# Optimization experiments

Hardware: AMD Instinct MI355X
Metric: run time of the kernel (lower is better)

The kernel has to match this reference:

```python
import jax, jax.numpy as jnp
import numpy as np

B, S, HID = 1, 8192, 768
H, D = 12, 64          # num heads, head dim (HID = H*D)
W = 256                # one-sided attention window


def _shift_chunks(xc, C):
    # xc: [B, C, w, H, D] -> prev/next chunk copies padded with zeros
    prev = jnp.pad(xc, ((0, 0), (1, 0), (0, 0), (0, 0), (0, 0)))[:, :C]
    nxt = jnp.pad(xc, ((0, 0), (0, 1), (0, 0), (0, 0), (0, 0)))[:, 1:]
    return jnp.concatenate([prev, xc, nxt], axis=2)  # [B, C, 3w, H, D]


def sliding_window_attention(q, k, v, w):
    # q,k,v: [B, S, H, D]; q already scaled. Band width 2w+1.
    b, s, h, d = q.shape
    c = s // w
    qc = q.reshape(b, c, w, h, d)
    k3 = _shift_chunks(k.reshape(b, c, w, h, d), c)  # [b,c,3w,h,d]
    v3 = _shift_chunks(v.reshape(b, c, w, h, d), c)
    # scores of each query chunk against its 3-chunk key neighborhood
    scores3 = jnp.einsum('bcxhd,bcyhd->bhcxy', qc, k3)  # [b,h,c,w,3w]
    rows = jnp.arange(w)
    offs = jnp.arange(2 * w + 1)
    gidx = rows[:, None] + offs[None, :]  # [w, 2w+1] local key index p+j
    band = scores3[..., rows[:, None], gidx]  # [b,h,c,w,2w+1]
    # mask keys outside [0, S) (same effect as mask_invalid_locations)
    gq = jnp.arange(s).reshape(c, w)                    # global query pos
    keypos = gq[..., None] + (offs - w)                 # [c,w,2w+1]
    valid = (keypos >= 0) & (keypos < s)
    band = jnp.where(valid[None, None], band, -jnp.inf)
    prob = jax.nn.softmax(band, axis=-1)
    prob = jnp.where(valid[None, None], prob, 0.0)
    # scatter band probs back to 3w layout, then banded PV matmul
    prob3 = jnp.zeros(band.shape[:-1] + (3 * w,), band.dtype)
    prob3 = prob3.at[..., rows[:, None], gidx].set(prob)  # [b,h,c,w,3w]
    ctx = jnp.einsum('bhcxy,bcyhd->bcxhd', prob3, v3)
    return ctx.reshape(b, s, h, d)


def setup_inputs() -> dict:
    key = jax.random.key(0)
    ks = jax.random.split(key, 4)
    sc = 1.0 / np.sqrt(HID)
    return {
        'hidden_states': jax.random.normal(ks[0], (B, S, HID), jnp.float32),
        'Wq': jax.random.normal(ks[1], (HID, HID), jnp.float32) * sc,
        'bq': jnp.zeros((HID,), jnp.float32),
        'Wk': jax.random.normal(ks[2], (HID, HID), jnp.float32) * sc,
        'bk': jnp.zeros((HID,), jnp.float32),
        'Wv': jax.random.normal(ks[3], (HID, HID), jnp.float32) * sc,
        'bv': jnp.zeros((HID,), jnp.float32),
    }


def reference(hidden_states, Wq, bq, Wk, bk, Wv, bv):
    b, s, hid = hidden_states.shape
    q = (hidden_states @ Wq + bq).reshape(b, s, H, D)
    k = (hidden_states @ Wk + bk).reshape(b, s, H, D)
    v = (hidden_states @ Wv + bv).reshape(b, s, H, D)
    q = q / jnp.asarray(np.sqrt(D), q.dtype)
    ctx = sliding_window_attention(q, k, v, W)  # [b,s,H,D]
    return ctx.reshape(b, s, hid)
```

## Files before the change

### kernel.cpp

```cpp
#include <hip/hip_runtime.h>
#include <hip/hip_bf16.h>

#define S_LEN 8192
#define HID 768
#define NH 12
#define HD 64
#define WIN 256

typedef __bf16 bf16x8 __attribute__((ext_vector_type(8)));
typedef float f32x4 __attribute__((ext_vector_type(4)));
using bf16_t = __hip_bfloat16;

#define MFMA(a, b, c) __builtin_amdgcn_mfma_f32_16x16x32_bf16(a, b, c, 0, 0, 0)

__device__ __forceinline__ void gl2lds16(const bf16_t* g, bf16_t* l) {
  __builtin_amdgcn_global_load_lds(
      (const __attribute__((address_space(1))) void*)g,
      (__attribute__((address_space(3))) void*)l, 16, 0, 0);
}

__global__ __launch_bounds__(256) void conv_hs(const float* __restrict__ hs,
                                               bf16_t* __restrict__ hb) {
  int i = (blockIdx.x * 256 + threadIdx.x) * 4;
  float4 v = *reinterpret_cast<const float4*>(hs + i);
  union { ushort4 u; bf16_t b[4]; } H;
  H.b[0] = __float2bfloat16(v.x);
  H.b[1] = __float2bfloat16(v.y);
  H.b[2] = __float2bfloat16(v.z);
  H.b[3] = __float2bfloat16(v.w);
  *reinterpret_cast<ushort4*>(hb + i) = H.u;
}

__global__ __launch_bounds__(256) void transpose_w(const float* __restrict__ Wq,
                                                   const float* __restrict__ Wk,
                                                   const float* __restrict__ Wv,
                                                   bf16_t* __restrict__ Wt) {
  __shared__ float t[32][33];
  int z = blockIdx.z;
  const float* src = (z == 0) ? Wq : ((z == 1) ? Wk : Wv);
  int n0 = blockIdx.x * 32, k0 = blockIdx.y * 32;
  int tx = threadIdx.x, ty = threadIdx.y;
  for (int i = 0; i < 4; ++i)
    t[ty + i * 8][tx] = src[(k0 + ty + i * 8) * HID + n0 + tx];
  __syncthreads();
  bf16_t* dst = Wt + z * HID * HID;
  for (int i = 0; i < 4; ++i)
    dst[(n0 + ty + i * 8) * HID + k0 + tx] = __float2bfloat16(t[tx][ty + i * 8]);
}

__global__ __launch_bounds__(256) void qkv_gemm(
    const bf16_t* __restrict__ hb, const bf16_t* __restrict__ Wt,
    const float* __restrict__ bq, const float* __restrict__ bk,
    const float* __restrict__ bv,
    bf16_t* __restrict__ Qw, bf16_t* __restrict__ Kw, bf16_t* __restrict__ Vt) {
  __shared__ __align__(16) bf16_t sA[128 * 64];
  __shared__ __align__(16) bf16_t sB[128 * 64];
  int m0 = blockIdx.x * 128;
  int zq = blockIdx.y / 6;
  int nn0 = (blockIdx.y % 6) * 128;
  int n0g = zq * HID + nn0;
  int tid = threadIdx.x;
  int w = tid >> 6, lane = tid & 63, lm = lane & 15, qd = lane >> 4;
  int wm = w & 1, wn = w >> 1;

  int srow = w * 8 + (lane >> 3);
  int sc8 = (lane & 7) ^ ((lane >> 3) & 7);
  const bf16_t* gA = hb + (m0 + srow) * HID + sc8 * 8;
  const bf16_t* gB = Wt + (n0g + srow) * HID + sc8 * 8;
  int sx0 = lm & 7;

  f32x4 acc[4][4] = {};
  for (int kk = 0; kk < HID; kk += 64) {
#pragma unroll
    for (int u = 0; u < 4; ++u) {
      gl2lds16(gA + (u * 32) * HID + kk, sA + u * 2048 + w * 512);
      gl2lds16(gB + (u * 32) * HID + kk, sB + u * 2048 + w * 512);
    }
    __syncthreads();
#pragma unroll
    for (int half = 0; half < 2; ++half) {
      int ca = (qd + 4 * half) ^ sx0;
      bf16x8 fa[4], fb[4];
#pragma unroll
      for (int i = 0; i < 4; ++i) {
        fa[i] = *reinterpret_cast<const bf16x8*>(
            sA + (wm * 64 + i * 16 + lm) * 64 + ca * 8);
        fb[i] = *reinterpret_cast<const bf16x8*>(
            sB + (wn * 64 + i * 16 + lm) * 64 + ca * 8);
      }
      if (zq == 2) {
#pragma unroll
        for (int i = 0; i < 4; ++i)
#pragma unroll
          for (int j = 0; j < 4; ++j)
            acc[i][j] = MFMA(fb[i], fa[j], acc[i][j]);
      } else {
#pragma unroll
        for (int i = 0; i < 4; ++i)
#pragma unroll
          for (int j = 0; j < 4; ++j)
            acc[i][j] = MFMA(fa[i], fb[j], acc[i][j]);
      }
    }
    __syncthreads();
  }

  if (zq != 2) {
    const float* bias = zq ? bk : bq;
    bf16_t* dst = zq ? Kw : Qw;
    float scale = zq ? 1.0f : 0.125f;
#pragma unroll
    for (int j = 0; j < 4; ++j) {
      int nl = nn0 + wn * 64 + j * 16 + lm;
      float bb = bias[nl];
      int h = nl >> 6, d = nl & 63;
#pragma unroll
      for (int i = 0; i < 4; ++i)
#pragma unroll
        for (int r = 0; r < 4; ++r) {
          int m = m0 + wm * 64 + i * 16 + qd * 4 + r;
          dst[(h * S_LEN + m) * HD + d] =
              __float2bfloat16((acc[i][j][r] + bb) * scale);
        }
    }
  } else {
#pragma unroll
    for (int i = 0; i < 4; ++i)
#pragma unroll
      for (int r = 0; r < 4; ++r) {
        int nl = nn0 + wn * 64 + i * 16 + qd * 4 + r;
        float bb = bv[nl];
#pragma unroll
        for (int j = 0; j < 4; ++j) {
          int m = m0 + wm * 64 + j * 16 + lm;
          Vt[nl * S_LEN + m] = __float2bfloat16(acc[i][j][r] + bb);
        }
      }
  }
}

__global__ __launch_bounds__(256) void swa_kernel(
    const bf16_t* __restrict__ Qw, const bf16_t* __restrict__ Kw,
    const bf16_t* __restrict__ Vt, float* __restrict__ out) {
  __shared__ __align__(16) bf16_t sK[2][64 * 64];
  __shared__ __align__(16) bf16_t sV[2][64 * 64];
  __shared__ __align__(16) bf16_t sP[4 * 16 * 72];
  int h = blockIdx.y;
  int nb = blockIdx.x;
  int q0 = (((nb & 7) << 4) | (nb >> 3)) * 64;
  int tid = threadIdx.x;
  int w = tid >> 6, lane = tid & 63, lm = lane & 15, qd = lane >> 4;
  int xb = q0 + w * 16;

  int qoff = (h * S_LEN + xb + lm) * HD + qd * 8;
  bf16x8 aq0 = *reinterpret_cast<const bf16x8*>(Qw + qoff);
  bf16x8 aq1 = *reinterpret_cast<const bf16x8*>(Qw + qoff + 32);

  f32x4 o[4] = {};
  float lsum[4] = {0.f, 0.f, 0.f, 0.f};

  int y_begin = q0 - WIN; if (y_begin < 0) y_begin = 0;
  int y_end = q0 + 64 + WIN; if (y_end > S_LEN) y_end = S_LEN;
  int ntiles = (y_end - y_begin) >> 6;
  const bf16_t* Kh = Kw + h * S_LEN * HD;
  const bf16_t* Vh = Vt + h * HD * S_LEN;
  bf16_t* sPw = sP + w * 16 * 72;

  int srow = w * 8 + (lane >> 3);
  int sc8 = (lane & 7) ^ ((lane >> 3) & 7);
  int sx0 = lm & 7;

#define STAGE(y0, b)                                                    \
  {                                                                     \
    const bf16_t* kg = Kh + ((y0) + srow) * HD + sc8 * 8;               \
    gl2lds16(kg, &sK[b][w * 512]);                                      \
    gl2lds16(kg + 32 * HD, &sK[b][2048 + w * 512]);                     \
    const bf16_t* vg = Vh + srow * S_LEN + (y0) + sc8 * 8;              \
    gl2lds16(vg, &sV[b][w * 512]);                                      \
    gl2lds16(vg + 32 * S_LEN, &sV[b][2048 + w * 512]);                  \
  }

  STAGE(y_begin, 0);
  __syncthreads();

  for (int t = 0; t < ntiles; ++t) {
    int y0 = y_begin + t * 64;
    if (t + 1 < ntiles) STAGE(y0 + 64, (t + 1) & 1);
    int b = t & 1;
    f32x4 s[4] = {};
#pragma unroll
    for (int nt = 0; nt < 4; ++nt) {
      const bf16_t* kr = &sK[b][(nt * 16 + lm) * 64];
      bf16x8 b0 = *reinterpret_cast<const bf16x8*>(kr + (qd ^ sx0) * 8);
      bf16x8 b1 = *reinterpret_cast<const bf16x8*>(kr + ((qd + 4) ^ sx0) * 8);
      s[nt] = MFMA(aq0, b0, s[nt]);
      s[nt] = MFMA(aq1, b1, s[nt]);
    }
    int dy = y0 - q0;
    bool edge = (dy > 192) || (dy < -192);
#pragma unroll
    for (int nt = 0; nt < 4; ++nt) {
#pragma unroll
      for (int r = 0; r < 4; ++r) {
        float pv;
        if (edge) {
          int dlt = (y0 + nt * 16 + lm) - (xb + qd * 4 + r);
          pv = (dlt <= WIN && dlt >= -WIN) ? __expf(s[nt][r]) : 0.f;
        } else {
          pv = __expf(s[nt][r]);
        }
        bf16_t pb = __float2bfloat16(pv);
        lsum[r] += __bfloat162float(pb);
        sPw[(qd * 4 + r) * 72 + nt * 16 + lm] = pb;
      }
    }
    bf16x8 ap0 = *reinterpret_cast<const bf16x8*>(sPw + lm * 72 + qd * 8);
    bf16x8 ap1 = *reinterpret_cast<const bf16x8*>(sPw + lm * 72 + 32 + qd * 8);
#pragma unroll
    for (int nt = 0; nt < 4; ++nt) {
      const bf16_t* vr = &sV[b][(nt * 16 + lm) * 64];
      bf16x8 v0 = *reinterpret_cast<const bf16x8*>(vr + (qd ^ sx0) * 8);
      bf16x8 v1 = *reinterpret_cast<const bf16x8*>(vr + ((qd + 4) ^ sx0) * 8);
      o[nt] = MFMA(ap0, v0, o[nt]);
      o[nt] = MFMA(ap1, v1, o[nt]);
    }
    __syncthreads();
  }
#pragma unroll
  for (int r = 0; r < 4; ++r) {
    float v = lsum[r];
    v += __shfl_xor(v, 1);
    v += __shfl_xor(v, 2);
    v += __shfl_xor(v, 4);
    v += __shfl_xor(v, 8);
    float inv = 1.f / v;
    int x = xb + qd * 4 + r;
#pragma unroll
    for (int nt = 0; nt < 4; ++nt)
      out[x * HID + h * HD + nt * 16 + lm] = o[nt][r] * inv;
  }
}

extern "C" void kernel_launch(void* const* d_in, const int* in_sizes, int n_in,
                              void* d_out, int out_size, void* d_ws, size_t ws_size,
                              hipStream_t stream) {
  const float* hs = (const float*)d_in[0];
  const float* Wq = (const float*)d_in[1];
  const float* bq = (const float*)d_in[2];
  const float* Wk = (const float*)d_in[3];
  const float* bk = (const float*)d_in[4];
  const float* Wv = (const float*)d_in[5];
  const float* bv = (const float*)d_in[6];
  float* out = (float*)d_out;

  const int NSH = S_LEN * HID;
  const int NW = 3 * HID * HID;
  bf16_t* p = (bf16_t*)d_ws;
  bf16_t* hb = p; p += NSH;
  bf16_t* Wt = p; p += NW;
  bf16_t* Qw = p; p += NSH;
  bf16_t* Kw = p; p += NSH;
  bf16_t* Vt = p; p += NSH;

  conv_hs<<<dim3(NSH / 4 / 256), dim3(256), 0, stream>>>(hs, hb);
  transpose_w<<<dim3(24, 24, 3), dim3(32, 8), 0, stream>>>(Wq, Wk, Wv, Wt);
  qkv_gemm<<<dim3(64, 18), dim3(256), 0, stream>>>(
      hb, Wt, bq, bk, bv, Qw, Kw, Vt);
  swa_kernel<<<dim3(128, 12), dim3(256), 0, stream>>>(Qw, Kw, Vt, out);
}
```

Before: 175.1 us.

## Merge prep kernels and transpose QK^T MFMA for vectorized P stores

Combines the hidden-state bf16 conversion and the weight transpose into one launch, which removes a kernel launch. In the attention kernel, the QK^T MFMA operands are swapped so each lane holds scores for one query row. This lets P be written to LDS as packed 4-element stores with an XOR swizzle instead of scalar stores with padding. The row sum becomes a single accumulator reduced across quads. It also adds a launch-bounds occupancy hint and sums unrounded fp32 probabilities, which changes numerics slightly.

```diff
diff --git a/kernel.cpp b/kernel.cpp
--- a/kernel.cpp
+++ b/kernel.cpp
@@ -19,27 +19,32 @@
       (__attribute__((address_space(3))) void*)l, 16, 0, 0);
 }
 
-__global__ __launch_bounds__(256) void conv_hs(const float* __restrict__ hs,
-                                               bf16_t* __restrict__ hb) {
-  int i = (blockIdx.x * 256 + threadIdx.x) * 4;
-  float4 v = *reinterpret_cast<const float4*>(hs + i);
-  union { ushort4 u; bf16_t b[4]; } H;
-  H.b[0] = __float2bfloat16(v.x);
-  H.b[1] = __float2bfloat16(v.y);
-  H.b[2] = __float2bfloat16(v.z);
-  H.b[3] = __float2bfloat16(v.w);
-  *reinterpret_cast<ushort4*>(hb + i) = H.u;
-}
-
-__global__ __launch_bounds__(256) void transpose_w(const float* __restrict__ Wq,
-                                                   const float* __restrict__ Wk,
-                                                   const float* __restrict__ Wv,
-                                                   bf16_t* __restrict__ Wt) {
+__global__ __launch_bounds__(256) void prep(const float* __restrict__ hs,
+                                            bf16_t* __restrict__ hb,
+                                            const float* __restrict__ Wq,
+                                            const float* __restrict__ Wk,
+                                            const float* __restrict__ Wv,
+                                            bf16_t* __restrict__ Wt) {
+  int bx = blockIdx.x;
+  int tid = threadIdx.x;
+  if (bx < 6144) {
+    int i = (bx * 256 + tid) * 4;
+    float4 v = *reinterpret_cast<const float4*>(hs + i);
+    union { ushort4 u; bf16_t b[4]; } H;
+    H.b[0] = __float2bfloat16(v.x);
+    H.b[1] = __float2bfloat16(v.y);
+    H.b[2] = __float2bfloat16(v.z);
+    H.b[3] = __float2bfloat16(v.w);
+    *reinterpret_cast<ushort4*>(hb + i) = H.u;
+    return;
+  }
   __shared__ float t[32][33];
-  int z = blockIdx.z;
+  int b = bx - 6144;
+  int z = b / 576;
+  int r = b % 576;
+  int n0 = (r / 24) * 32, k0 = (r % 24) * 32;
   const float* src = (z == 0) ? Wq : ((z == 1) ? Wk : Wv);
-  int n0 = blockIdx.x * 32, k0 = blockIdx.y * 32;
-  int tx = threadIdx.x, ty = threadIdx.y;
+  int tx = tid & 31, ty = tid >> 5;
   for (int i = 0; i < 4; ++i)
     t[ty + i * 8][tx] = src[(k0 + ty + i * 8) * HID + n0 + tx];
   __syncthreads();
@@ -139,12 +144,12 @@
   }
 }
 
-__global__ __launch_bounds__(256) void swa_kernel(
+__global__ __launch_bounds__(256, 4) void swa_kernel(
     const bf16_t* __restrict__ Qw, const bf16_t* __restrict__ Kw,
     const bf16_t* __restrict__ Vt, float* __restrict__ out) {
   __shared__ __align__(16) bf16_t sK[2][64 * 64];
   __shared__ __align__(16) bf16_t sV[2][64 * 64];
-  __shared__ __align__(16) bf16_t sP[4 * 16 * 72];
+  __shared__ __align__(16) bf16_t sP[4 * 16 * 64];
   int h = blockIdx.y;
   int nb = blockIdx.x;
   int q0 = (((nb & 7) << 4) | (nb >> 3)) * 64;
@@ -157,14 +162,14 @@
   bf16x8 aq1 = *reinterpret_cast<const bf16x8*>(Qw + qoff + 32);
 
   f32x4 o[4] = {};
-  float lsum[4] = {0.f, 0.f, 0.f, 0.f};
+  float lsum = 0.f;
 
   int y_begin = q0 - WIN; if (y_begin < 0) y_begin = 0;
   int y_end = q0 + 64 + WIN; if (y_end > S_LEN) y_end = S_LEN;
   int ntiles = (y_end - y_begin) >> 6;
   const bf16_t* Kh = Kw + h * S_LEN * HD;
   const bf16_t* Vh = Vt + h * HD * S_LEN;
-  bf16_t* sPw = sP + w * 16 * 72;
+  bf16_t* sPw = sP + w * 16 * 64;
 
   int srow = w * 8 + (lane >> 3);
   int sc8 = (lane & 7) ^ ((lane >> 3) & 7);
@@ -193,29 +198,34 @@
       const bf16_t* kr = &sK[b][(nt * 16 + lm) * 64];
       bf16x8 b0 = *reinterpret_cast<const bf16x8*>(kr + (qd ^ sx0) * 8);
       bf16x8 b1 = *reinterpret_cast<const bf16x8*>(kr + ((qd + 4) ^ sx0) * 8);
-      s[nt] = MFMA(aq0, b0, s[nt]);
-      s[nt] = MFMA(aq1, b1, s[nt]);
+      s[nt] = MFMA(b0, aq0, s[nt]);
+      s[nt] = MFMA(b1, aq1, s[nt]);
     }
     int dy = y0 - q0;
     bool edge = (dy > 192) || (dy < -192);
 #pragma unroll
     for (int nt = 0; nt < 4; ++nt) {
+      union { ushort4 u; bf16_t b[4]; } P;
 #pragma unroll
       for (int r = 0; r < 4; ++r) {
         float pv;
         if (edge) {
-          int dlt = (y0 + nt * 16 + lm) - (xb + qd * 4 + r);
+          int dlt = (y0 + nt * 16 + qd * 4 + r) - (xb + lm);
           pv = (dlt <= WIN && dlt >= -WIN) ? __expf(s[nt][r]) : 0.f;
         } else {
           pv = __expf(s[nt][r]);
         }
-        bf16_t pb = __float2bfloat16(pv);
-        lsum[r] += __bfloat162float(pb);
-        sPw[(qd * 4 + r) * 72 + nt * 16 + lm] = pb;
-      }
-    }
-    bf16x8 ap0 = *reinterpret_cast<const bf16x8*>(sPw + lm * 72 + qd * 8);
-    bf16x8 ap1 = *reinterpret_cast<const bf16x8*>(sPw + lm * 72 + 32 + qd * 8);
+        lsum += pv;
+        P.b[r] = __float2bfloat16(pv);
+      }
+      *reinterpret_cast<ushort4*>(
+          sPw + lm * 64 + (((2 * nt + (qd >> 1)) ^ sx0) * 8) + (qd & 1) * 4) =
+          P.u;
+    }
+    bf16x8 ap0 =
+        *reinterpret_cast<const bf16x8*>(sPw + lm * 64 + ((qd ^ sx0) * 8));
+    bf16x8 ap1 = *reinterpret_cast<const bf16x8*>(sPw + lm * 64 +
+                                                  (((qd + 4) ^ sx0) * 8));
 #pragma unroll
     for (int nt = 0; nt < 4; ++nt) {
       const bf16_t* vr = &sV[b][(nt * 16 + lm) * 64];
@@ -226,14 +236,11 @@
     }
     __syncthreads();
   }
+  lsum += __shfl_xor(lsum, 16);
+  lsum += __shfl_xor(lsum, 32);
 #pragma unroll
   for (int r = 0; r < 4; ++r) {
-    float v = lsum[r];
-    v += __shfl_xor(v, 1);
-    v += __shfl_xor(v, 2);
-    v += __shfl_xor(v, 4);
-    v += __shfl_xor(v, 8);
-    float inv = 1.f / v;
+    float inv = 1.f / __shfl(lsum, qd * 4 + r);
     int x = xb + qd * 4 + r;
 #pragma unroll
     for (int nt = 0; nt < 4; ++nt)
@@ -262,8 +269,7 @@
   bf16_t* Kw = p; p += NSH;
   bf16_t* Vt = p; p += NSH;
 
-  conv_hs<<<dim3(NSH / 4 / 256), dim3(256), 0, stream>>>(hs, hb);
-  transpose_w<<<dim3(24, 24, 3), dim3(32, 8), 0, stream>>>(Wq, Wk, Wv, Wt);
+  prep<<<dim3(6144 + 1728), dim3(256), 0, stream>>>(hs, hb, Wq, Wk, Wv, Wt);
   qkv_gemm<<<dim3(64, 18), dim3(256), 0, stream>>>(
       hb, Wt, bq, bk, bv, Qw, Kw, Vt);
   swa_kernel<<<dim3(128, 12), dim3(256), 0, stream>>>(Qw, Kw, Vt, out);
```

Result: faster. 166.2 us (-5.1%).
